# Kernel tuning notes

Measured on AMD Instinct MI355X. Metric: run time of the kernel, lower is better.

The kernel has to match this reference:

```python
import jax, jax.numpy as jnp
import numpy as np

N = 10000      # nodes
E = 160000     # edges (before self-loops)
IN = 256
NEG_SLOPE = 0.2  # PyG GATConv default


def gat_layer(x, src, dst, W, a_src, a_dst, bias, heads, concat, n):
    # x: [n, in_dim]; W: [in_dim, heads*C]; a_src/a_dst: [heads, C]
    C = W.shape[1] // heads
    h = (x @ W).reshape(n, heads, C)                      # [n,H,C]
    es = jnp.einsum('nhc,hc->nh', h, a_src)               # [n,H]
    ed = jnp.einsum('nhc,hc->nh', h, a_dst)               # [n,H]
    e = jax.nn.leaky_relu(es[src] + ed[dst], NEG_SLOPE)   # [E,H]
    # segment softmax over destination node (every node has a self-loop)
    emax = jax.ops.segment_max(e, dst, num_segments=n)    # [n,H]
    al = jnp.exp(e - emax[dst])                           # [E,H]
    den = jax.ops.segment_sum(al, dst, num_segments=n)    # [n,H]
    al = al / den[dst]
    out = jax.ops.segment_sum(h[src] * al[:, :, None], dst, num_segments=n)  # [n,H,C]
    out = out.reshape(n, heads * C) if concat else out.mean(axis=1)
    return out + bias


def setup_inputs() -> dict:
    key = jax.random.key(0)
    ks = jax.random.split(key, 16)
    s = 0.05
    p = lambda k, shp: jax.random.normal(k, shp, dtype=jnp.float32) * s
    return {
        'x': jax.random.normal(ks[0], (N, IN), dtype=jnp.float32),
        'edge_index': jax.random.randint(ks[1], (2, E), 0, N, dtype=jnp.int64),
        'proj_w': p(ks[2], (IN, 512)), 'proj_b': jnp.zeros((512,), jnp.float32),
        'w1': p(ks[3], (512, 4 * 512)),  'as1': p(ks[4], (4, 512)), 'ad1': p(ks[5], (4, 512)),  'b1': jnp.zeros((2048,), jnp.float32),
        'w2': p(ks[6], (2048, 4 * 512)), 'as2': p(ks[7], (4, 512)), 'ad2': p(ks[8], (4, 512)),  'b2': jnp.zeros((2048,), jnp.float32),
        'w3': p(ks[9], (2048, 2 * 512)), 'as3': p(ks[10], (2, 512)), 'ad3': p(ks[11], (2, 512)), 'b3': jnp.zeros((512,), jnp.float32),
    }


def reference(x, edge_index, proj_w, proj_b, w1, as1, ad1, b1,
              w2, as2, ad2, b2, w3, as3, ad3, b3):
    n = x.shape[0]
    loops = jnp.arange(n, dtype=edge_index.dtype)
    src = jnp.concatenate([edge_index[0], loops])   # PyG add_self_loops=True
    dst = jnp.concatenate([edge_index[1], loops])
    h = x @ proj_w + proj_b                         # dropout is identity in eval
    h = gat_layer(h, src, dst, w1, as1, ad1, b1, 4, True, n)
    h = jax.nn.elu(h)
    h = gat_layer(h, src, dst, w2, as2, ad2, b2, 4, True, n)
    h = jax.nn.elu(h)
    h = gat_layer(h, src, dst, w3, as3, ad3, b3, 2, False, n)
    return h
```

## Files before the change

kernel.cpp:

```cpp
#include <hip/hip_runtime.h>
#include <hip/hip_bf16.h>
#include <math.h>

#define CDIV(a,b) (((a)+(b)-1)/(b))

typedef __bf16  bf16x8 __attribute__((ext_vector_type(8)));
typedef float   f32x4  __attribute__((ext_vector_type(4)));
typedef unsigned short u16x8 __attribute__((ext_vector_type(8)));
typedef unsigned short u16x4 __attribute__((ext_vector_type(4)));

__device__ __forceinline__ float bf2f(unsigned short u) {
    union { unsigned int i; float f; } x; x.i = ((unsigned int)u) << 16; return x.f;
}
__device__ __forceinline__ unsigned short f2bf(float f) {
    union { float f; unsigned int i; } x; x.f = f;
    unsigned int r = x.i + 0x7fff + ((x.i >> 16) & 1);
    return (unsigned short)(r >> 16);
}

__device__ __forceinline__ void bfx8_cvt(u16x8 v, float f[8]) {
    union { u16x8 v; unsigned d[4]; } u; u.v = v;
#pragma unroll
    for (int q = 0; q < 4; q++) {
        f[2*q]   = __uint_as_float(u.d[q] << 16);
        f[2*q+1] = __uint_as_float(u.d[q] & 0xffff0000u);
    }
}
__device__ __forceinline__ void bfx4_cvt(u16x4 v, float f[4]) {
    union { u16x4 v; unsigned d[2]; } u; u.v = v;
#pragma unroll
    for (int q = 0; q < 2; q++) {
        f[2*q]   = __uint_as_float(u.d[q] << 16);
        f[2*q+1] = __uint_as_float(u.d[q] & 0xffff0000u);
    }
}
__device__ __forceinline__ float elu_fast(float v) {
    return (v > 0.f) ? v : (__expf(v) - 1.f);
}

__global__ void hist_kernel(const int* __restrict__ ei, int* __restrict__ deg,
                            int E, int Et) {
    int e = blockIdx.x * blockDim.x + threadIdx.x;
    if (e >= Et) return;
    int d = (e < E) ? ei[E + e] : (e - E);
    atomicAdd(&deg[d], 1);
}

__global__ void scan_kernel(const int* __restrict__ deg, int* __restrict__ off, int n) {
    __shared__ int wsum[16];
    __shared__ int carry_s;
    int t = threadIdx.x, lane = t & 63, wv = t >> 6;
    if (t == 0) carry_s = 0;
    __syncthreads();
    for (int base = 0; base < n; base += 1024) {
        int v = (base + t < n) ? deg[base + t] : 0;
        int x = v;
#pragma unroll
        for (int o = 1; o < 64; o <<= 1) {
            int y = __shfl_up(x, o);
            if (lane >= o) x += y;
        }
        if (lane == 63) wsum[wv] = x;
        __syncthreads();
        if (wv == 0 && lane < 16) {
            int s = wsum[lane];
#pragma unroll
            for (int o = 1; o < 16; o <<= 1) {
                int y = __shfl_up(s, o);
                if (lane >= o) s += y;
            }
            wsum[lane] = s;
        }
        __syncthreads();
        int wprev = (wv == 0) ? 0 : wsum[wv - 1];
        int incl = carry_s + wprev + x;
        if (base + t < n) off[base + t] = incl - v;
        __syncthreads();
        if (t == 1023) carry_s = incl;
        __syncthreads();
    }
    if (t == 0) off[n] = carry_s;
}

__global__ void scatter_kernel(const int* __restrict__ ei, const int* __restrict__ off,
                               int* __restrict__ cur, int* __restrict__ csr,
                               int E, int Et) {
    int e = blockIdx.x * blockDim.x + threadIdx.x;
    if (e >= Et) return;
    int s, d;
    if (e < E) { s = ei[e]; d = ei[E + e]; } else { s = e - E; d = s; }
    int pos = off[d] + atomicAdd(&cur[d], 1);
    csr[pos] = s;
}

__global__ void prep_t_kernel(const float* __restrict__ wa, __hip_bfloat16* __restrict__ wta,
                              const float* __restrict__ wb, __hip_bfloat16* __restrict__ wtb,
                              const float* __restrict__ wc, __hip_bfloat16* __restrict__ wtc,
                              int t0, int t1, int t2) {
    __shared__ float tile[32][33];
    int bid = blockIdx.x;
    const float* w; __hip_bfloat16* wt; int K, N, r;
    if (bid < t0)      { w = wa; wt = wta; K = 512;  N = 2048; r = bid; }
    else if (bid < t1) { w = wb; wt = wtb; K = 2048; N = 2048; r = bid - t0; }
    else               { w = wc; wt = wtc; K = 2048; N = 1024; r = bid - t1; }
    (void)t2;
    int kt = K >> 5;
    int kb = (r % kt) * 32, nb = (r / kt) * 32;
    int tx = threadIdx.x & 31, ty = threadIdx.x >> 5;
    for (int i = ty; i < 32; i += 8)
        tile[i][tx] = w[(size_t)(kb + i) * N + nb + tx];
    __syncthreads();
    for (int i = ty; i < 32; i += 8)
        wt[(size_t)(nb + i) * K + kb + tx] = __float2bfloat16(tile[tx][i]);
}

__global__ void cvt2_kernel(const float* __restrict__ a, __hip_bfloat16* __restrict__ ao,
                            int na4,
                            const float* __restrict__ b, __hip_bfloat16* __restrict__ bo,
                            int nb4) {
    int i = blockIdx.x * blockDim.x + threadIdx.x;
    const float* src; __hip_bfloat16* dst; int idx;
    if (i < na4) { src = a; dst = ao; idx = i * 4; }
    else if (i < na4 + nb4) { src = b; dst = bo; idx = (i - na4) * 4; }
    else return;
    float4 v = *(const float4*)(src + idx);
    dst[idx + 0] = __float2bfloat16(v.x);
    dst[idx + 1] = __float2bfloat16(v.y);
    dst[idx + 2] = __float2bfloat16(v.z);
    dst[idx + 3] = __float2bfloat16(v.w);
}

__global__ void beff_kernel(const float* __restrict__ pb, const float* __restrict__ w1,
                            float* __restrict__ beff, int N) {
    int j  = blockIdx.x * 256 + threadIdx.x;
    int k0 = blockIdx.y * 64;
    float s = 0.f;
#pragma unroll
    for (int k = 0; k < 64; k++)
        s = fmaf(pb[k0 + k], w1[(size_t)(k0 + k) * N + j], s);
    atomicAdd(&beff[j], s);
}

__global__ void va_kernel(const __hip_bfloat16* __restrict__ w_efft,
                          const float* __restrict__ b_eff,
                          const float* __restrict__ as1, const float* __restrict__ ad1,
                          const float* __restrict__ b1,
                          float* __restrict__ va, float* __restrict__ cvec,
                          float* __restrict__ b1s) {
    int j = blockIdx.x, t = threadIdx.x;
    if (j == 8) {
        for (int i = t; i < 2048; i += 256) b1s[i] = b_eff[i] + b1[i];
        return;
    }
    int h = j & 3;
    const float* a = ((j < 4) ? as1 : ad1) + h * 512;
    __shared__ float aLDS[512];
    __shared__ float red[256];
    for (int c = t; c < 512; c += 256) aLDS[c] = a[c];
    __syncthreads();
    float acc = 0.f;
    const unsigned short* wb = (const unsigned short*)w_efft + (size_t)h * 512 * 256 + t;
    for (int c = 0; c < 512; c++)
        acc = fmaf(aLDS[c], bf2f(wb[(size_t)c * 256]), acc);
    va[j * 256 + t] = acc;
    float cp = b_eff[h * 512 + t] * aLDS[t] + b_eff[h * 512 + 256 + t] * aLDS[256 + t];
    red[t] = cp;
    __syncthreads();
    for (int s = 128; s > 0; s >>= 1) {
        if (t < s) red[t] += red[t + s];
        __syncthreads();
    }
    if (t == 0) cvec[j] = red[0];
}

__global__ void es1_kernel(const __hip_bfloat16* __restrict__ x_bf,
                           const float* __restrict__ va, const float* __restrict__ cvec,
                           float* __restrict__ es, float* __restrict__ ed) {
    int node = blockIdx.x, l = threadIdx.x;
    u16x4 xv = *(const u16x4*)((const unsigned short*)x_bf + (size_t)node * 256 + l * 4);
    float xf[4];
    bfx4_cvt(xv, xf);
    float dot[8];
#pragma unroll
    for (int j = 0; j < 8; j++) {
        float4 v = *(const float4*)(va + j * 256 + l * 4);
        dot[j] = xf[0] * v.x + xf[1] * v.y + xf[2] * v.z + xf[3] * v.w;
    }
#pragma unroll
    for (int j = 0; j < 8; j++)
        for (int o = 32; o; o >>= 1) dot[j] += __shfl_down(dot[j], o);
    if (l == 0) {
#pragma unroll
        for (int h = 0; h < 4; h++) {
            es[node * 4 + h] = dot[h] + cvec[h];
            ed[node * 4 + h] = dot[4 + h] + cvec[4 + h];
        }
    }
}

__global__ __launch_bounds__(256) void alpha4_kernel(
    const float* __restrict__ es, const float* __restrict__ ed,
    const int* __restrict__ csr, const int* __restrict__ off,
    float4* __restrict__ al4, int n)
{
    int d = blockIdx.x * 4 + (threadIdx.x >> 6);
    if (d >= n) return;
    int lane = threadIdx.x & 63;
    int beg = off[d], end = off[d + 1];
    float edd[4], den[4];
#pragma unroll
    for (int h = 0; h < 4; h++) { edd[h] = ed[d * 4 + h]; den[h] = 0.f; }
    for (int i = beg + lane; i < end; i += 64) {
        int s = csr[i];
#pragma unroll
        for (int h = 0; h < 4; h++) {
            float e = es[s * 4 + h] + edd[h];
            e = (e > 0.f) ? e : 0.2f * e;
            den[h] += __expf(e);
        }
    }
#pragma unroll
    for (int h = 0; h < 4; h++) {
        for (int o = 32; o; o >>= 1) den[h] += __shfl_down(den[h], o);
        den[h] = __shfl(den[h], 0);
        den[h] = 1.f / den[h];
    }
    for (int i = beg + lane; i < end; i += 64) {
        int s = csr[i];
        float a[4];
#pragma unroll
        for (int h = 0; h < 4; h++) {
            float e = es[s * 4 + h] + edd[h];
            e = (e > 0.f) ? e : 0.2f * e;
            a[h] = __expf(e) * den[h];
        }
        al4[i] = make_float4(a[0], a[1], a[2], a[3]);
    }
}

__global__ __launch_bounds__(256) void agg1x_kernel(
    const __hip_bfloat16* __restrict__ x_bf, const float4* __restrict__ al4,
    const int* __restrict__ csr, const int* __restrict__ off,
    __hip_bfloat16* __restrict__ z)
{
    __shared__ float red[4][1024];
    int d = blockIdx.x, t = threadIdx.x;
    int w = t >> 6, l = t & 63;
    int c0 = l * 4;
    int beg = off[d], end = off[d + 1];
    float acc[4][4] = {};
    const unsigned short* xb = (const unsigned short*)x_bf;

    for (int i = beg + w; i < end; i += 4) {
        int s = csr[i];
        float4 a = al4[i];
        u16x4 xv = *(const u16x4*)(xb + (size_t)s * 256 + c0);
        float xf[4];
        bfx4_cvt(xv, xf);
#pragma unroll
        for (int k = 0; k < 4; k++) {
            acc[k][0] = fmaf(a.x, xf[k], acc[k][0]);
            acc[k][1] = fmaf(a.y, xf[k], acc[k][1]);
            acc[k][2] = fmaf(a.z, xf[k], acc[k][2]);
            acc[k][3] = fmaf(a.w, xf[k], acc[k][3]);
        }
    }
#pragma unroll
    for (int h = 0; h < 4; h++)
#pragma unroll
        for (int k = 0; k < 4; k++)
            red[w][h * 256 + c0 + k] = acc[k][h];
    __syncthreads();
    unsigned short* zb = (unsigned short*)z + (size_t)d * 1024;
#pragma unroll
    for (int q = 0; q < 4; q++) {
        int m = t + q * 256;
        float v = red[0][m] + red[1][m] + red[2][m] + red[3][m];
        zb[m] = f2bf(v);
    }
}

__device__ __forceinline__ void gload16(void* lds, const void* g) {
    __builtin_amdgcn_global_load_lds(
        (const __attribute__((address_space(1))) void*)g,
        (__attribute__((address_space(3))) void*)lds, 16, 0, 0);
}

__global__ __launch_bounds__(256) void gemm_bf16_kernel(
    const __hip_bfloat16* __restrict__ A,
    const __hip_bfloat16* __restrict__ BT,
    const float* __restrict__ bias,
    __hip_bfloat16* __restrict__ Cb,
    int M, int N, int K, int lda, int hko, int do_elu,
    int MB, int NB, int XT, int NBH)
{
    __shared__ __align__(16) __hip_bfloat16 As[128 * 32];
    __shared__ __align__(16) __hip_bfloat16 Bs[128 * 32];

    const int bid  = blockIdx.x;
    const int xcd  = bid & 7;
    const int slot = bid >> 3;
    const int per_yh = XT * NBH;
    const int yh    = slot / per_yh;
    const int rem   = slot - yh * per_yh;
    const int x_sub = rem / NBH;
    const int ys    = rem - x_sub * NBH;
    const int yb    = yh * NBH + ys;
    const int xb    = xcd * XT + x_sub;
    if (xb >= MB || yb >= NB) return;

    const int tid = threadIdx.x;
    const int m0 = xb * 128, n0 = yb * 128;
    const int w = tid >> 6, l = tid & 63;
    const int wm = (w & 1) * 64, wn = (w >> 1) * 64;
    const int lm = l & 15, lq = l >> 4;

    f32x4 acc[4][4] = {};

    const int arow = tid >> 2;
    const int acol = (tid & 3) * 8;
    const __hip_bfloat16* Ag = A + (size_t)(m0 + arow) * lda + acol + (n0 >> 9) * hko;
    const __hip_bfloat16* Bg = BT + (size_t)(n0 + arow) * K + acol;
    char* AsW = (char*)As + (w << 10);
    char* BsW = (char*)Bs + (w << 10);

    for (int k0 = 0; k0 < K; k0 += 32) {
        gload16(AsW,        Ag + k0);
        gload16(AsW + 4096, Ag + (size_t)64 * lda + k0);
        gload16(BsW,        Bg + k0);
        gload16(BsW + 4096, Bg + (size_t)64 * K + k0);
        __syncthreads();
        bf16x8 af[4], bfr[4];
#pragma unroll
        for (int i = 0; i < 4; i++)
            af[i] = *(const bf16x8*)(As + (wm + i * 16 + lm) * 32 + lq * 8);
#pragma unroll
        for (int j = 0; j < 4; j++)
            bfr[j] = *(const bf16x8*)(Bs + (wn + j * 16 + lm) * 32 + lq * 8);
#pragma unroll
        for (int i = 0; i < 4; i++)
#pragma unroll
            for (int j = 0; j < 4; j++)
                acc[i][j] = __builtin_amdgcn_mfma_f32_16x16x32_bf16(
                    af[i], bfr[j], acc[i][j], 0, 0, 0);
        __syncthreads();
    }

#pragma unroll
    for (int i = 0; i < 4; i++) {
        int rb = m0 + wm + i * 16 + lq * 4;
#pragma unroll
        for (int r = 0; r < 4; r++) {
            int row = rb + r;
            if (row >= M) continue;
#pragma unroll
            for (int j = 0; j < 4; j++) {
                int col = n0 + wn + j * 16 + lm;
                float v = acc[i][j][r];
                if (bias) v += bias[col];
                if (do_elu) v = elu_fast(v);
                Cb[(size_t)row * N + col] = __float2bfloat16(v);
            }
        }
    }
}

__global__ __launch_bounds__(512, 2) void gemm256_kernel(
    const __hip_bfloat16* __restrict__ A,
    const __hip_bfloat16* __restrict__ BT,
    __hip_bfloat16* __restrict__ Cb,
    int M, int N, int K, int MT, int nfull)
{
    __shared__ __align__(16) char smem[131072];
    const int NT = K >> 6;

    const int cpx  = gridDim.x >> 3;
    const int bid  = blockIdx.x;
    const int slot = (bid & 7) * cpx + (bid >> 3);
    int mt, ntl;
    if (slot < nfull) { mt = slot % MT; ntl = slot / MT; }
    else              { ntl = nfull / MT; mt = (nfull % MT) + (slot - nfull); }
    const int m0 = mt << 8, n0 = ntl << 8;

    const int tid = threadIdx.x;
    const int w  = tid >> 6, l = tid & 63;
    const int wr = w >> 2, wc = w & 3;
    const int lm = l & 15, lq = l >> 4;

    const int srow = tid >> 3;
    const int scol = ((l & 7) << 3) ^ ((l >> 3) << 3);
    const __hip_bfloat16* As0 = A  + (size_t)(m0 + srow) * K + scol;
    const __hip_bfloat16* Bs0 = BT + (size_t)(n0 + srow) * K + scol;
    const size_t rs64  = (size_t)64  * K;
    const size_t rs128 = (size_t)128 * K;
    char* const stA = smem +          ((size_t)w << 10);
    char* const stB = smem + 65536 +  ((size_t)w << 10);

    auto STAGE_A = [&](int par, int hf, int tt) {
        char* d = stA + (((par << 1) | hf) << 14);
        const __hip_bfloat16* s = As0 + (size_t)hf * rs128 + (tt << 6);
        gload16(d,        s);
        gload16(d + 8192, s + rs64);
    };
    auto STAGE_B = [&](int par, int hf, int tt) {
        char* d = stB + (((par << 1) | hf) << 14);
        const __hip_bfloat16* s = Bs0 + (size_t)hf * rs128 + (tt << 6);
        gload16(d,        s);
        gload16(d + 8192, s + rs64);
    };

    const int roff = lm << 7;
    const int xm   = (lm & 7) << 4;
    const int off0 = (lq << 4) ^ xm;
    const int off1 = off0 ^ 64;
    const int bsel = 65536 + ((wc & 1) << 13);

    f32x4  acc[8][4] = {};
    bf16x8 af[8][2];
    bf16x8 bfr[2][2];

    STAGE_A(0, 0, 0); STAGE_A(0, 1, 0);
    STAGE_B(0, 0, 0); STAGE_B(0, 1, 0);
    STAGE_A(1, 0, 1); STAGE_A(1, 1, 1);
    asm volatile("s_waitcnt vmcnt(4)" ::: "memory");
    __builtin_amdgcn_s_barrier();

    for (int t = 0; t < NT; ++t) {
        const int par = t & 1;
        const char* aS = smem + (((par << 1) | wr)        << 14) + roff;
        const char* bS = smem + (((par << 1) | (wc >> 1)) << 14) + bsel + roff;

#pragma unroll
        for (int i = 0; i < 4; ++i) {
            af[i][0] = *(const bf16x8*)(aS + i * 2048 + off0);
            af[i][1] = *(const bf16x8*)(aS + i * 2048 + off1);
        }
#pragma unroll
        for (int j = 0; j < 2; ++j) {
            bfr[j][0] = *(const bf16x8*)(bS + j * 2048 + off0);
            bfr[j][1] = *(const bf16x8*)(bS + j * 2048 + off1);
        }
        if (t + 1 < NT) STAGE_B(par ^ 1, 0, t + 1);
        __builtin_amdgcn_s_barrier();
        asm volatile("s_waitcnt lgkmcnt(0)" ::: "memory");
        __builtin_amdgcn_sched_barrier(0);
        __builtin_amdgcn_s_setprio(1);
#pragma unroll
        for (int i = 0; i < 4; ++i)
#pragma unroll
            for (int j = 0; j < 2; ++j) {
                acc[i][j] = __builtin_amdgcn_mfma_f32_16x16x32_bf16(af[i][0], bfr[j][0], acc[i][j], 0, 0, 0);
                acc[i][j] = __builtin_amdgcn_mfma_f32_16x16x32_bf16(af[i][1], bfr[j][1], acc[i][j], 0, 0, 0);
            }
        __builtin_amdgcn_s_setprio(0);
        __builtin_amdgcn_s_barrier();

#pragma unroll
        for (int i = 4; i < 8; ++i) {
            af[i][0] = *(const bf16x8*)(aS + i * 2048 + off0);
            af[i][1] = *(const bf16x8*)(aS + i * 2048 + off1);
        }
        if (t + 1 < NT) STAGE_B(par ^ 1, 1, t + 1);
        __builtin_amdgcn_s_barrier();
        asm volatile("s_waitcnt lgkmcnt(0)" ::: "memory");
        __builtin_amdgcn_sched_barrier(0);
        __builtin_amdgcn_s_setprio(1);
#pragma unroll
        for (int i = 4; i < 8; ++i)
#pragma unroll
            for (int j = 0; j < 2; ++j) {
                acc[i][j] = __builtin_amdgcn_mfma_f32_16x16x32_bf16(af[i][0], bfr[j][0], acc[i][j], 0, 0, 0);
                acc[i][j] = __builtin_amdgcn_mfma_f32_16x16x32_bf16(af[i][1], bfr[j][1], acc[i][j], 0, 0, 0);
            }
        __builtin_amdgcn_s_setprio(0);
        __builtin_amdgcn_s_barrier();

#pragma unroll
        for (int j = 0; j < 2; ++j) {
            bfr[j][0] = *(const bf16x8*)(bS + (j + 2) * 2048 + off0);
            bfr[j][1] = *(const bf16x8*)(bS + (j + 2) * 2048 + off1);
        }
        if (t + 2 < NT) STAGE_A(par, 0, t + 2);
        __builtin_amdgcn_s_barrier();
        asm volatile("s_waitcnt lgkmcnt(0)" ::: "memory");
        __builtin_amdgcn_sched_barrier(0);
        __builtin_amdgcn_s_setprio(1);
#pragma unroll
        for (int i = 0; i < 4; ++i)
#pragma unroll
            for (int j = 0; j < 2; ++j) {
                acc[i][j + 2] = __builtin_amdgcn_mfma_f32_16x16x32_bf16(af[i][0], bfr[j][0], acc[i][j + 2], 0, 0, 0);
                acc[i][j + 2] = __builtin_amdgcn_mfma_f32_16x16x32_bf16(af[i][1], bfr[j][1], acc[i][j + 2], 0, 0, 0);
            }
        __builtin_amdgcn_s_setprio(0);
        __builtin_amdgcn_s_barrier();

        if (t + 2 < NT) STAGE_A(par, 1, t + 2);
        __builtin_amdgcn_s_barrier();
        __builtin_amdgcn_sched_barrier(0);
        __builtin_amdgcn_s_setprio(1);
#pragma unroll
        for (int i = 4; i < 8; ++i)
#pragma unroll
            for (int j = 0; j < 2; ++j) {
                acc[i][j + 2] = __builtin_amdgcn_mfma_f32_16x16x32_bf16(af[i][0], bfr[j][0], acc[i][j + 2], 0, 0, 0);
                acc[i][j + 2] = __builtin_amdgcn_mfma_f32_16x16x32_bf16(af[i][1], bfr[j][1], acc[i][j + 2], 0, 0, 0);
            }
        __builtin_amdgcn_s_setprio(0);
        if (t + 2 < NT)      { asm volatile("s_waitcnt vmcnt(4)" ::: "memory"); }
        else if (t + 1 < NT) { asm volatile("s_waitcnt vmcnt(0)" ::: "memory"); }
        __builtin_amdgcn_s_barrier();
    }

#pragma unroll
    for (int i = 0; i < 8; ++i) {
        int rb = m0 + wr * 128 + i * 16 + lq * 4;
#pragma unroll
        for (int r = 0; r < 4; ++r) {
            int row = rb + r;
            if (row >= M) continue;
#pragma unroll
            for (int j = 0; j < 4; ++j) {
                int col = n0 + wc * 64 + j * 16 + lm;
                Cb[(size_t)row * N + col] = __float2bfloat16(acc[i][j][r]);
            }
        }
    }
}

__global__ __launch_bounds__(256, 2) void gemm128_kernel(
    const __hip_bfloat16* __restrict__ A,
    const __hip_bfloat16* __restrict__ BT,
    __hip_bfloat16* __restrict__ Cb,
    int M, int N, int K, int mode, int RT)
{
    __shared__ __align__(16) char smem[65536];
    const int NT = K >> 6;

    const int cpx  = gridDim.x >> 3;
    const int bid  = blockIdx.x;
    const int slot = (bid & 7) * cpx + (bid >> 3);
    int r, c;
    if (mode == 0) { r = slot % RT; c = slot / RT; }
    else {
        if (slot < 96) { c = 12 + slot / 48; r = 32 + slot % 48; }
        else           { int u = slot - 96; c = 14 + u / 80; r = u % 80; }
    }
    const int m0 = r << 7, n0 = c << 7;

    const int tid = threadIdx.x;
    const int w = tid >> 6, l = tid & 63;
    const int wm = (w & 1) << 6, wn = (w >> 1) << 6;
    const int lm = l & 15, lq = l >> 4;

    const int srow = tid >> 3;
    const int scol = (((tid & 7) ^ ((tid >> 3) & 7)) << 3);
    const __hip_bfloat16* Ag = A  + (size_t)(m0 + srow) * K + scol;
    const __hip_bfloat16* Bg = BT + (size_t)(n0 + srow) * K + scol;
    const size_t rs32 = (size_t)32 * K;
    char* const dA = smem +         ((size_t)w << 10);
    char* const dB = smem + 16384 + ((size_t)w << 10);

    auto STAGE = [&](int par, int tt) {
        char* pa = dA + (par << 15);
        char* pb = dB + (par << 15);
        const __hip_bfloat16* sa = Ag + (tt << 6);
        const __hip_bfloat16* sb = Bg + (tt << 6);
#pragma unroll
        for (int s = 0; s < 4; ++s) {
            gload16(pa + (s << 12), sa + (size_t)s * rs32);
            gload16(pb + (s << 12), sb + (size_t)s * rs32);
        }
    };

    const int roff = lm << 7;
    const int off0 = (lq << 4) ^ ((lm & 7) << 4);
    const int off1 = off0 ^ 64;

    f32x4 acc[4][4] = {};

    STAGE(0, 0);
    asm volatile("s_waitcnt vmcnt(0)" ::: "memory");
    __builtin_amdgcn_s_barrier();

    for (int t = 0; t < NT; ++t) {
        const int par = t & 1;
        if (t + 1 < NT) STAGE(par ^ 1, t + 1);
        const char* aS = smem + (par << 15) +         wm * 128 + roff;
        const char* bS = smem + (par << 15) + 16384 + wn * 128 + roff;
        bf16x8 af[4][2], bfr[4][2];
#pragma unroll
        for (int i = 0; i < 4; ++i) {
            af[i][0]  = *(const bf16x8*)(aS + i * 2048 + off0);
            af[i][1]  = *(const bf16x8*)(aS + i * 2048 + off1);
            bfr[i][0] = *(const bf16x8*)(bS + i * 2048 + off0);
            bfr[i][1] = *(const bf16x8*)(bS + i * 2048 + off1);
        }
        asm volatile("s_waitcnt lgkmcnt(0)" ::: "memory");
        __builtin_amdgcn_sched_barrier(0);
        __builtin_amdgcn_s_setprio(1);
#pragma unroll
        for (int i = 0; i < 4; ++i)
#pragma unroll
            for (int j = 0; j < 4; ++j) {
                acc[i][j] = __builtin_amdgcn_mfma_f32_16x16x32_bf16(af[i][0], bfr[j][0], acc[i][j], 0, 0, 0);
                acc[i][j] = __builtin_amdgcn_mfma_f32_16x16x32_bf16(af[i][1], bfr[j][1], acc[i][j], 0, 0, 0);
            }
        __builtin_amdgcn_s_setprio(0);
        if (t + 1 < NT) asm volatile("s_waitcnt vmcnt(0)" ::: "memory");
        __builtin_amdgcn_s_barrier();
    }

#pragma unroll
    for (int i = 0; i < 4; ++i) {
        int rb = m0 + wm + i * 16 + lq * 4;
#pragma unroll
        for (int r2 = 0; r2 < 4; ++r2) {
            int row = rb + r2;
            if (row >= M) continue;
#pragma unroll
            for (int j = 0; j < 4; ++j) {
                int col = n0 + wn + j * 16 + lm;
                Cb[(size_t)row * N + col] = __float2bfloat16(acc[i][j][r2]);
            }
        }
    }
}

__global__ void esed_kernel(const __hip_bfloat16* __restrict__ h,
                            const float* __restrict__ a_src,
                            const float* __restrict__ a_dst,
                            float* __restrict__ es, float* __restrict__ ed, int H) {
    int nidx = blockIdx.x;
    int t = threadIdx.x;
    int head = t >> 6, lane = t & 63;
    const unsigned short* hp =
        (const unsigned short*)h + (size_t)nidx * H * 512 + head * 512 + lane * 8;
    const float* sp = a_src + head * 512 + lane * 8;
    const float* dp = a_dst + head * 512 + lane * 8;
    u16x8 hv = *(const u16x8*)hp;
    float4 s0 = *(const float4*)sp, s1 = *(const float4*)(sp + 4);
    float4 d0 = *(const float4*)dp, d1 = *(const float4*)(dp + 4);
    float hf[8];
    bfx8_cvt(hv, hf);
    float s = hf[0]*s0.x + hf[1]*s0.y + hf[2]*s0.z + hf[3]*s0.w
            + hf[4]*s1.x + hf[5]*s1.y + hf[6]*s1.z + hf[7]*s1.w;
    float d = hf[0]*d0.x + hf[1]*d0.y + hf[2]*d0.z + hf[3]*d0.w
            + hf[4]*d1.x + hf[5]*d1.y + hf[6]*d1.z + hf[7]*d1.w;
    for (int o = 32; o; o >>= 1) { s += __shfl_down(s, o); d += __shfl_down(d, o); }
    if (lane == 0) { es[nidx * H + head] = s; ed[nidx * H + head] = d; }
}

template<int H, int SHIFT>
__global__ __launch_bounds__(256) void alpharec_kernel(
    const float* __restrict__ es, const float* __restrict__ ed,
    const int* __restrict__ csr, const int* __restrict__ off,
    uint2* __restrict__ rec, int n)
{
    int d = blockIdx.x * 4 + (threadIdx.x >> 6);
    if (d >= n) return;
    int lane = threadIdx.x & 63;
    int beg = off[d], end = off[d + 1];
    float edd[H], den[H];
#pragma unroll
    for (int h = 0; h < H; h++) { edd[h] = ed[d * H + h]; den[h] = 0.f; }
    for (int i = beg + lane; i < end; i += 64) {
        int s = csr[i];
#pragma unroll
        for (int h = 0; h < H; h++) {
            float e = es[s * H + h] + edd[h];
            e = (e > 0.f) ? e : 0.2f * e;
            den[h] += __expf(e);
        }
    }
#pragma unroll
    for (int h = 0; h < H; h++) {
        for (int o = 32; o; o >>= 1) den[h] += __shfl_down(den[h], o);
        den[h] = __shfl(den[h], 0);
        den[h] = 1.f / den[h];
    }
    for (int i = beg + lane; i < end; i += 64) {
        int s = csr[i];
        unsigned obytes = ((unsigned)s) << SHIFT;
#pragma unroll
        for (int h = 0; h < H; h++) {
            float e = es[s * H + h] + edd[h];
            e = (e > 0.f) ? e : 0.2f * e;
            float a = __expf(e) * den[h];
            rec[(size_t)i * H + h] = make_uint2(obytes, __float_as_uint(a));
        }
    }
}

__global__ __launch_bounds__(256) void agg2s_kernel(
    const __hip_bfloat16* __restrict__ h, const uint2* __restrict__ rec,
    const int* __restrict__ off, const float* __restrict__ bias,
    __hip_bfloat16* __restrict__ outB, int n)
{
    const int bid   = blockIdx.x;
    const int slice = bid & 7;
    const int head  = slice >> 1;
    const int wvs   = (bid >> 3) * 4 + (threadIdx.x >> 6);
    const int lane  = threadIdx.x & 63;
    const int half  = lane >> 5;
    const int c0    = slice * 256 + (lane & 31) * 8;
    const unsigned c0b = (unsigned)c0 * 2;
    const char* hb = (const char*)h;
    float bv[8];
#pragma unroll
    for (int k = 0; k < 8; k++) bv[k] = bias[c0 + k];

    for (int d = wvs; d < n; d += 1024) {
        int beg = off[d], end = off[d + 1];
        float acc[8] = {0.f, 0.f, 0.f, 0.f, 0.f, 0.f, 0.f, 0.f};
        int i = beg + half;
        for (; i + 2 < end; i += 4) {
            uint2 r0 = rec[i * 4 + head];
            uint2 r1 = rec[(i + 2) * 4 + head];
            u16x8 v0 = *(const u16x8*)(hb + (size_t)(r0.x + c0b));
            u16x8 v1 = *(const u16x8*)(hb + (size_t)(r1.x + c0b));
            float a0 = __uint_as_float(r0.y);
            float a1 = __uint_as_float(r1.y);
            float f0[8], f1[8];
            bfx8_cvt(v0, f0);
            bfx8_cvt(v1, f1);
#pragma unroll
            for (int k = 0; k < 8; k++) acc[k] = fmaf(a0, f0[k], acc[k]);
#pragma unroll
            for (int k = 0; k < 8; k++) acc[k] = fmaf(a1, f1[k], acc[k]);
        }
        for (; i < end; i += 2) {
            uint2 r0 = rec[i * 4 + head];
            u16x8 v0 = *(const u16x8*)(hb + (size_t)(r0.x + c0b));
            float a0 = __uint_as_float(r0.y);
            float f0[8];
            bfx8_cvt(v0, f0);
#pragma unroll
            for (int k = 0; k < 8; k++) acc[k] = fmaf(a0, f0[k], acc[k]);
        }
#pragma unroll
        for (int k = 0; k < 8; k++) acc[k] += __shfl_xor(acc[k], 32);
        if (half == 0) {
            u16x8 ov;
#pragma unroll
            for (int k = 0; k < 8; k++) {
                float v = elu_fast(acc[k] + bv[k]);
                ov[k] = f2bf(v);
            }
            *(u16x8*)((unsigned short*)outB + (size_t)d * 2048 + c0) = ov;
        }
    }
}

__global__ __launch_bounds__(256) void agg3s_kernel(
    const __hip_bfloat16* __restrict__ h, const uint2* __restrict__ rec,
    const int* __restrict__ off, float* __restrict__ part, int n)
{
    const int bid   = blockIdx.x;
    const int xcd   = bid & 7;
    const int slice = xcd >> 1;
    const int head  = slice >> 1;
    const int sb    = ((bid >> 3) << 1) | (xcd & 1);
    const int wvs   = sb * 4 + (threadIdx.x >> 6);
    const int lane  = threadIdx.x & 63;
    const int half  = lane >> 5;
    const int c0    = slice * 256 + (lane & 31) * 8;
    const unsigned c0b = (unsigned)c0 * 2;
    const char* hb = (const char*)h;

    for (int d = wvs; d < n; d += 2048) {
        int beg = off[d], end = off[d + 1];
        float acc[8] = {0.f, 0.f, 0.f, 0.f, 0.f, 0.f, 0.f, 0.f};
        int i = beg + half;
        for (; i + 2 < end; i += 4) {
            uint2 r0 = rec[i * 2 + head];
            uint2 r1 = rec[(i + 2) * 2 + head];
            u16x8 v0 = *(const u16x8*)(hb + (size_t)(r0.x + c0b));
            u16x8 v1 = *(const u16x8*)(hb + (size_t)(r1.x + c0b));
            float a0 = __uint_as_float(r0.y);
            float a1 = __uint_as_float(r1.y);
            float f0[8], f1[8];
            bfx8_cvt(v0, f0);
            bfx8_cvt(v1, f1);
#pragma unroll
            for (int k = 0; k < 8; k++) acc[k] = fmaf(a0, f0[k], acc[k]);
#pragma unroll
            for (int k = 0; k < 8; k++) acc[k] = fmaf(a1, f1[k], acc[k]);
        }
        for (; i < end; i += 2) {
            uint2 r0 = rec[i * 2 + head];
            u16x8 v0 = *(const u16x8*)(hb + (size_t)(r0.x + c0b));
            float a0 = __uint_as_float(r0.y);
            float f0[8];
            bfx8_cvt(v0, f0);
#pragma unroll
            for (int k = 0; k < 8; k++) acc[k] = fmaf(a0, f0[k], acc[k]);
        }
#pragma unroll
        for (int k = 0; k < 8; k++) acc[k] += __shfl_xor(acc[k], 32);
        if (half == 0) {
            float* pp = part + (size_t)d * 1024 + c0;
            *(float4*)pp       = make_float4(acc[0], acc[1], acc[2], acc[3]);
            *(float4*)(pp + 4) = make_float4(acc[4], acc[5], acc[6], acc[7]);
        }
    }
}

__global__ void comb3_kernel(const float* __restrict__ part,
                             const float* __restrict__ b3,
                             float* __restrict__ out, int n) {
    int idx = blockIdx.x * 256 + threadIdx.x;
    if (idx >= n * 128) return;
    int d = idx >> 7, c = (idx & 127) * 4;
    float4 p0 = *(const float4*)(part + (size_t)d * 1024 + c);
    float4 p1 = *(const float4*)(part + (size_t)d * 1024 + 512 + c);
    float4 bb = *(const float4*)(b3 + c);
    float4 o;
    o.x = 0.5f * (p0.x + p1.x) + bb.x;
    o.y = 0.5f * (p0.y + p1.y) + bb.y;
    o.z = 0.5f * (p0.z + p1.z) + bb.z;
    o.w = 0.5f * (p0.w + p1.w) + bb.w;
    *(float4*)(out + (size_t)d * 512 + c) = o;
}

extern "C" void kernel_launch(void* const* d_in, const int* in_sizes, int n_in,
                              void* d_out, int out_size, void* d_ws, size_t ws_size,
                              hipStream_t stream) {
    const float* x      = (const float*)d_in[0];
    const int*   ei     = (const int*)  d_in[1];
    const float* proj_w = (const float*)d_in[2];
    const float* proj_b = (const float*)d_in[3];
    const float* w1  = (const float*)d_in[4];
    const float* as1 = (const float*)d_in[5];
    const float* ad1 = (const float*)d_in[6];
    const float* b1  = (const float*)d_in[7];
    const float* w2  = (const float*)d_in[8];
    const float* as2 = (const float*)d_in[9];
    const float* ad2 = (const float*)d_in[10];
    const float* b2  = (const float*)d_in[11];
    const float* w3  = (const float*)d_in[12];
    const float* as3 = (const float*)d_in[13];
    const float* ad3 = (const float*)d_in[14];
    const float* b3  = (const float*)d_in[15];

    const int n    = in_sizes[0] / 256;
    const int E    = in_sizes[1] / 2;
    const int Et   = E + n;
    const int MB   = CDIV(n, 128);
    const int MB2  = CDIV(n, 256);
    const int Mpad = MB2 * 256;
    const int XT   = CDIV(MB, 8);

    char* p = (char*)d_ws;
    auto carve = [&](size_t bytes) {
        void* r = (void*)p;
        p += (bytes + 255) & ~(size_t)255;
        return r;
    };
    __hip_bfloat16* h_bf    = (__hip_bfloat16*)carve((size_t)Mpad * 2048 * sizeof(__hip_bfloat16));
    __hip_bfloat16* act_bf  = (__hip_bfloat16*)carve((size_t)Mpad * 2048 * sizeof(__hip_bfloat16));
    __hip_bfloat16* x_bf    = (__hip_bfloat16*)carve((size_t)Mpad * 256 * sizeof(__hip_bfloat16));
    __hip_bfloat16* pw_bf   = (__hip_bfloat16*)carve((size_t)256 * 512 * sizeof(__hip_bfloat16));
    __hip_bfloat16* w1t     = (__hip_bfloat16*)carve((size_t)2048 * 512 * sizeof(__hip_bfloat16));
    __hip_bfloat16* w2t     = (__hip_bfloat16*)carve((size_t)2048 * 2048 * sizeof(__hip_bfloat16));
    __hip_bfloat16* w3t     = (__hip_bfloat16*)carve((size_t)1024 * 2048 * sizeof(__hip_bfloat16));
    __hip_bfloat16* w_efft  = (__hip_bfloat16*)carve((size_t)2048 * 256 * sizeof(__hip_bfloat16));
    float* b_eff = (float*)carve((size_t)2048 * sizeof(float));
    float* b1s   = (float*)carve((size_t)2048 * sizeof(float));
    float* va    = (float*)carve((size_t)8 * 256 * sizeof(float));
    float* cvec  = (float*)carve((size_t)8 * sizeof(float));
    float* es  = (float*)carve((size_t)n * 4 * sizeof(float));
    float* ed  = (float*)carve((size_t)n * 4 * sizeof(float));
    uint2* rec = (uint2*)carve((size_t)Et * 4 * sizeof(uint2));
    int* deg = (int*)carve((size_t)2 * n * sizeof(int));
    int* cur = deg + n;
    int* off = (int*)carve((size_t)(n + 1) * sizeof(int));
    int* csr = (int*)carve((size_t)Et * sizeof(int));
    __hip_bfloat16* z_bf = h_bf;
    float* part = (float*)act_bf;
    float4* al4 = (float4*)rec;
    (void)ws_size; (void)n_in;

    hipMemsetAsync(deg, 0, 2 * n * sizeof(int), stream);
    hipMemsetAsync(b_eff, 0, 2048 * sizeof(float), stream);
    hist_kernel<<<CDIV(Et, 256), 256, 0, stream>>>(ei, deg, E, Et);
    scan_kernel<<<1, 1024, 0, stream>>>(deg, off, n);
    scatter_kernel<<<CDIV(Et, 256), 256, 0, stream>>>(ei, off, cur, csr, E, Et);

    const int t0 = (512 / 32) * (2048 / 32);
    const int t1 = t0 + (2048 / 32) * (2048 / 32);
    const int t2 = t1 + (2048 / 32) * (1024 / 32);
    prep_t_kernel<<<t2, 256, 0, stream>>>(w1, w1t, w2, w2t, w3, w3t, t0, t1, t2);
    const int na4 = 256 * 512 / 4, nb4 = n * 256 / 4;
    cvt2_kernel<<<CDIV(na4 + nb4, 256), 256, 0, stream>>>(proj_w, pw_bf, na4, x, x_bf, nb4);

    gemm_bf16_kernel<<<8 * 2 * 2, 256, 0, stream>>>(
        w1t, pw_bf, nullptr, w_efft, 2048, 256, 512, 512, 0, 0, 16, 2, 2, 2);
    beff_kernel<<<dim3(2048 / 256, 512 / 64), 256, 0, stream>>>(proj_b, w1, b_eff, 2048);

    va_kernel<<<9, 256, 0, stream>>>(w_efft, b_eff, as1, ad1, b1, va, cvec, b1s);

    es1_kernel<<<n, 64, 0, stream>>>(x_bf, va, cvec, es, ed);
    alpha4_kernel<<<CDIV(n, 4), 256, 0, stream>>>(es, ed, csr, off, al4, n);
    agg1x_kernel<<<n, 256, 0, stream>>>(x_bf, al4, csr, off, z_bf);
    gemm_bf16_kernel<<<8 * XT * 16, 256, 0, stream>>>(
        z_bf, w_efft, b1s, act_bf, n, 2048, 256, 1024, 256, 1, MB, 16, XT, 16);

    gemm256_kernel<<<256, 512, 0, stream>>>(act_bf, w2t, h_bf, n, 2048, 2048, 40, 240);
    gemm128_kernel<<<256, 256, 0, stream>>>(act_bf, w2t, h_bf, n, 2048, 2048, 1, 0);
    esed_kernel<<<n, 4 * 64, 0, stream>>>(h_bf, as2, ad2, es, ed, 4);
    alpharec_kernel<4, 12><<<CDIV(n, 4), 256, 0, stream>>>(es, ed, csr, off, rec, n);
    agg2s_kernel<<<2048, 256, 0, stream>>>(h_bf, rec, off, b2, act_bf, n);

    gemm128_kernel<<<640, 256, 0, stream>>>(act_bf, w3t, h_bf, n, 1024, 2048, 0, 80);
    esed_kernel<<<n, 2 * 64, 0, stream>>>(h_bf, as3, ad3, es, ed, 2);
    alpharec_kernel<2, 11><<<CDIV(n, 4), 256, 0, stream>>>(es, ed, csr, off, rec, n);
    agg3s_kernel<<<2048, 256, 0, stream>>>(h_bf, rec, off, part, n);
    comb3_kernel<<<CDIV(n * 128, 256), 256, 0, stream>>>(part, b3, (float*)d_out, n);
}
```

Measured before the change: 572.7 us.

## Fuse layer-1 softmax into aggregation and fold head-mean into layer-3 aggregation

Removes the separate alpha4 kernel: agg1x now computes the per-destination softmax denominator with a block reduction and recomputes the attention weights inline, so the float4 alpha array is never written or read back. In layer 3, each wave now accumulates both heads for its output columns, applies the 0.5 mean and bias, and writes the final output directly. This drops the partial buffer and the comb3 kernel. The costs are recomputed exps, doubled gather work per wave in agg3, and a changed grid mapping that drops the XCD-aware slicing, with the grid-stride loop now stepping by 4096.

```diff
diff --git a/kernel.cpp b/kernel.cpp
--- a/kernel.cpp
+++ b/kernel.cpp
@@ -198,71 +198,67 @@
     }
 }
 
-__global__ __launch_bounds__(256) void alpha4_kernel(
-    const float* __restrict__ es, const float* __restrict__ ed,
-    const int* __restrict__ csr, const int* __restrict__ off,
-    float4* __restrict__ al4, int n)
-{
-    int d = blockIdx.x * 4 + (threadIdx.x >> 6);
-    if (d >= n) return;
-    int lane = threadIdx.x & 63;
-    int beg = off[d], end = off[d + 1];
-    float edd[4], den[4];
-#pragma unroll
-    for (int h = 0; h < 4; h++) { edd[h] = ed[d * 4 + h]; den[h] = 0.f; }
-    for (int i = beg + lane; i < end; i += 64) {
-        int s = csr[i];
-#pragma unroll
-        for (int h = 0; h < 4; h++) {
-            float e = es[s * 4 + h] + edd[h];
-            e = (e > 0.f) ? e : 0.2f * e;
-            den[h] += __expf(e);
-        }
-    }
-#pragma unroll
-    for (int h = 0; h < 4; h++) {
-        for (int o = 32; o; o >>= 1) den[h] += __shfl_down(den[h], o);
-        den[h] = __shfl(den[h], 0);
-        den[h] = 1.f / den[h];
-    }
-    for (int i = beg + lane; i < end; i += 64) {
-        int s = csr[i];
-        float a[4];
-#pragma unroll
-        for (int h = 0; h < 4; h++) {
-            float e = es[s * 4 + h] + edd[h];
-            e = (e > 0.f) ? e : 0.2f * e;
-            a[h] = __expf(e) * den[h];
-        }
-        al4[i] = make_float4(a[0], a[1], a[2], a[3]);
-    }
-}
-
 __global__ __launch_bounds__(256) void agg1x_kernel(
-    const __hip_bfloat16* __restrict__ x_bf, const float4* __restrict__ al4,
-    const int* __restrict__ csr, const int* __restrict__ off,
-    __hip_bfloat16* __restrict__ z)
+    const __hip_bfloat16* __restrict__ x_bf, const float* __restrict__ es,
+    const float* __restrict__ ed, const int* __restrict__ csr,
+    const int* __restrict__ off, __hip_bfloat16* __restrict__ z)
 {
     __shared__ float red[4][1024];
+    __shared__ float denS[4][4];
     int d = blockIdx.x, t = threadIdx.x;
     int w = t >> 6, l = t & 63;
     int c0 = l * 4;
     int beg = off[d], end = off[d + 1];
+    float4 edv = *(const float4*)(ed + d * 4);
+    float edd[4] = {edv.x, edv.y, edv.z, edv.w};
+
+    float den[4] = {0.f, 0.f, 0.f, 0.f};
+    for (int i = beg + t; i < end; i += 256) {
+        int s = csr[i];
+        float4 ev = *(const float4*)(es + s * 4);
+        float e0 = ev.x + edd[0]; e0 = (e0 > 0.f) ? e0 : 0.2f * e0;
+        float e1 = ev.y + edd[1]; e1 = (e1 > 0.f) ? e1 : 0.2f * e1;
+        float e2 = ev.z + edd[2]; e2 = (e2 > 0.f) ? e2 : 0.2f * e2;
+        float e3 = ev.w + edd[3]; e3 = (e3 > 0.f) ? e3 : 0.2f * e3;
+        den[0] += __expf(e0); den[1] += __expf(e1);
+        den[2] += __expf(e2); den[3] += __expf(e3);
+    }
+#pragma unroll
+    for (int h = 0; h < 4; h++)
+        for (int o = 32; o; o >>= 1) den[h] += __shfl_down(den[h], o);
+    if (l == 0) {
+#pragma unroll
+        for (int h = 0; h < 4; h++) denS[w][h] = den[h];
+    }
+    __syncthreads();
+    float inv[4];
+#pragma unroll
+    for (int h = 0; h < 4; h++)
+        inv[h] = 1.f / (denS[0][h] + denS[1][h] + denS[2][h] + denS[3][h]);
+
     float acc[4][4] = {};
     const unsigned short* xb = (const unsigned short*)x_bf;
-
     for (int i = beg + w; i < end; i += 4) {
         int s = csr[i];
-        float4 a = al4[i];
+        float4 ev = *(const float4*)(es + s * 4);
+        float a[4];
+        {
+            float e0 = ev.x + edd[0]; e0 = (e0 > 0.f) ? e0 : 0.2f * e0;
+            float e1 = ev.y + edd[1]; e1 = (e1 > 0.f) ? e1 : 0.2f * e1;
+            float e2 = ev.z + edd[2]; e2 = (e2 > 0.f) ? e2 : 0.2f * e2;
+            float e3 = ev.w + edd[3]; e3 = (e3 > 0.f) ? e3 : 0.2f * e3;
+            a[0] = __expf(e0) * inv[0]; a[1] = __expf(e1) * inv[1];
+            a[2] = __expf(e2) * inv[2]; a[3] = __expf(e3) * inv[3];
+        }
         u16x4 xv = *(const u16x4*)(xb + (size_t)s * 256 + c0);
         float xf[4];
         bfx4_cvt(xv, xf);
 #pragma unroll
         for (int k = 0; k < 4; k++) {
-            acc[k][0] = fmaf(a.x, xf[k], acc[k][0]);
-            acc[k][1] = fmaf(a.y, xf[k], acc[k][1]);
-            acc[k][2] = fmaf(a.z, xf[k], acc[k][2]);
-            acc[k][3] = fmaf(a.w, xf[k], acc[k][3]);
+            acc[k][0] = fmaf(a[0], xf[k], acc[k][0]);
+            acc[k][1] = fmaf(a[1], xf[k], acc[k][1]);
+            acc[k][2] = fmaf(a[2], xf[k], acc[k][2]);
+            acc[k][3] = fmaf(a[3], xf[k], acc[k][3]);
         }
     }
 #pragma unroll
@@ -754,73 +750,75 @@
 
 __global__ __launch_bounds__(256) void agg3s_kernel(
     const __hip_bfloat16* __restrict__ h, const uint2* __restrict__ rec,
-    const int* __restrict__ off, float* __restrict__ part, int n)
+    const int* __restrict__ off, const float* __restrict__ b3,
+    float* __restrict__ out, int n)
 {
     const int bid   = blockIdx.x;
-    const int xcd   = bid & 7;
-    const int slice = xcd >> 1;
-    const int head  = slice >> 1;
-    const int sb    = ((bid >> 3) << 1) | (xcd & 1);
+    const int slice = bid & 1;
+    const int sb    = bid >> 1;
     const int wvs   = sb * 4 + (threadIdx.x >> 6);
     const int lane  = threadIdx.x & 63;
     const int half  = lane >> 5;
     const int c0    = slice * 256 + (lane & 31) * 8;
     const unsigned c0b = (unsigned)c0 * 2;
     const char* hb = (const char*)h;
-
-    for (int d = wvs; d < n; d += 2048) {
+    float bv[8];
+#pragma unroll
+    for (int k = 0; k < 8; k++) bv[k] = b3[c0 + k];
+
+    for (int d = wvs; d < n; d += 4096) {
         int beg = off[d], end = off[d + 1];
         float acc[8] = {0.f, 0.f, 0.f, 0.f, 0.f, 0.f, 0.f, 0.f};
         int i = beg + half;
         for (; i + 2 < end; i += 4) {
-            uint2 r0 = rec[i * 2 + head];
-            uint2 r1 = rec[(i + 2) * 2 + head];
-            u16x8 v0 = *(const u16x8*)(hb + (size_t)(r0.x + c0b));
-            u16x8 v1 = *(const u16x8*)(hb + (size_t)(r1.x + c0b));
-            float a0 = __uint_as_float(r0.y);
-            float a1 = __uint_as_float(r1.y);
-            float f0[8], f1[8];
-            bfx8_cvt(v0, f0);
-            bfx8_cvt(v1, f1);
-#pragma unroll
-            for (int k = 0; k < 8; k++) acc[k] = fmaf(a0, f0[k], acc[k]);
-#pragma unroll
-            for (int k = 0; k < 8; k++) acc[k] = fmaf(a1, f1[k], acc[k]);
+            uint4 r0 = *(const uint4*)(rec + (size_t)i * 2);
+            uint4 r1 = *(const uint4*)(rec + (size_t)(i + 2) * 2);
+            u16x8 v00 = *(const u16x8*)(hb + (size_t)(r0.x + c0b));
+            u16x8 v01 = *(const u16x8*)(hb + (size_t)(r0.x + 1024 + c0b));
+            u16x8 v10 = *(const u16x8*)(hb + (size_t)(r1.x + c0b));
+            u16x8 v11 = *(const u16x8*)(hb + (size_t)(r1.x + 1024 + c0b));
+            float a00 = __uint_as_float(r0.y), a01 = __uint_as_float(r0.w);
+            float a10 = __uint_as_float(r1.y), a11 = __uint_as_float(r1.w);
+            float f[8];
+            bfx8_cvt(v00, f);
+#pragma unroll
+            for (int k = 0; k < 8; k++) acc[k] = fmaf(a00, f[k], acc[k]);
+            bfx8_cvt(v01, f);
+#pragma unroll
+            for (int k = 0; k < 8; k++) acc[k] = fmaf(a01, f[k], acc[k]);
+            bfx8_cvt(v10, f);
+#pragma unroll
+            for (int k = 0; k < 8; k++) acc[k] = fmaf(a10, f[k], acc[k]);
+            bfx8_cvt(v11, f);
+#pragma unroll
+            for (int k = 0; k < 8; k++) acc[k] = fmaf(a11, f[k], acc[k]);
         }
         for (; i < end; i += 2) {
-            uint2 r0 = rec[i * 2 + head];
-            u16x8 v0 = *(const u16x8*)(hb + (size_t)(r0.x + c0b));
-            float a0 = __uint_as_float(r0.y);
-            float f0[8];
-            bfx8_cvt(v0, f0);
-#pragma unroll
-            for (int k = 0; k < 8; k++) acc[k] = fmaf(a0, f0[k], acc[k]);
+            uint4 r0 = *(const uint4*)(rec + (size_t)i * 2);
+            u16x8 v00 = *(const u16x8*)(hb + (size_t)(r0.x + c0b));
+            u16x8 v01 = *(const u16x8*)(hb + (size_t)(r0.x + 1024 + c0b));
+            float a00 = __uint_as_float(r0.y), a01 = __uint_as_float(r0.w);
+            float f[8];
+            bfx8_cvt(v00, f);
+#pragma unroll
+            for (int k = 0; k < 8; k++) acc[k] = fmaf(a00, f[k], acc[k]);
+            bfx8_cvt(v01, f);
+#pragma unroll
+            for (int k = 0; k < 8; k++) acc[k] = fmaf(a01, f[k], acc[k]);
         }
 #pragma unroll
         for (int k = 0; k < 8; k++) acc[k] += __shfl_xor(acc[k], 32);
         if (half == 0) {
-            float* pp = part + (size_t)d * 1024 + c0;
-            *(float4*)pp       = make_float4(acc[0], acc[1], acc[2], acc[3]);
-            *(float4*)(pp + 4) = make_float4(acc[4], acc[5], acc[6], acc[7]);
-        }
-    }
-}
-
-__global__ void comb3_kernel(const float* __restrict__ part,
-                             const float* __restrict__ b3,
-                             float* __restrict__ out, int n) {
-    int idx = blockIdx.x * 256 + threadIdx.x;
-    if (idx >= n * 128) return;
-    int d = idx >> 7, c = (idx & 127) * 4;
-    float4 p0 = *(const float4*)(part + (size_t)d * 1024 + c);
-    float4 p1 = *(const float4*)(part + (size_t)d * 1024 + 512 + c);
-    float4 bb = *(const float4*)(b3 + c);
-    float4 o;
-    o.x = 0.5f * (p0.x + p1.x) + bb.x;
-    o.y = 0.5f * (p0.y + p1.y) + bb.y;
-    o.z = 0.5f * (p0.z + p1.z) + bb.z;
-    o.w = 0.5f * (p0.w + p1.w) + bb.w;
-    *(float4*)(out + (size_t)d * 512 + c) = o;
+            float* op = out + (size_t)d * 512 + c0;
+            float4 o0, o1;
+            o0.x = 0.5f * acc[0] + bv[0]; o0.y = 0.5f * acc[1] + bv[1];
+            o0.z = 0.5f * acc[2] + bv[2]; o0.w = 0.5f * acc[3] + bv[3];
+            o1.x = 0.5f * acc[4] + bv[4]; o1.y = 0.5f * acc[5] + bv[5];
+            o1.z = 0.5f * acc[6] + bv[6]; o1.w = 0.5f * acc[7] + bv[7];
+            *(float4*)op       = o0;
+            *(float4*)(op + 4) = o1;
+        }
+    }
 }
 
 extern "C" void kernel_launch(void* const* d_in, const int* in_sizes, int n_in,
@@ -877,8 +875,6 @@
     int* off = (int*)carve((size_t)(n + 1) * sizeof(int));
     int* csr = (int*)carve((size_t)Et * sizeof(int));
     __hip_bfloat16* z_bf = h_bf;
-    float* part = (float*)act_bf;
-    float4* al4 = (float4*)rec;
     (void)ws_size; (void)n_in;
 
     hipMemsetAsync(deg, 0, 2 * n * sizeof(int), stream);
@@ -901,8 +897,7 @@
     va_kernel<<<9, 256, 0, stream>>>(w_efft, b_eff, as1, ad1, b1, va, cvec, b1s);
 
     es1_kernel<<<n, 64, 0, stream>>>(x_bf, va, cvec, es, ed);
-    alpha4_kernel<<<CDIV(n, 4), 256, 0, stream>>>(es, ed, csr, off, al4, n);
-    agg1x_kernel<<<n, 256, 0, stream>>>(x_bf, al4, csr, off, z_bf);
+    agg1x_kernel<<<n, 256, 0, stream>>>(x_bf, es, ed, csr, off, z_bf);
     gemm_bf16_kernel<<<8 * XT * 16, 256, 0, stream>>>(
         z_bf, w_efft, b1s, act_bf, n, 2048, 256, 1024, 256, 1, MB, 16, XT, 16);
 
@@ -915,6 +910,5 @@
     gemm128_kernel<<<640, 256, 0, stream>>>(act_bf, w3t, h_bf, n, 1024, 2048, 0, 80);
     esed_kernel<<<n, 2 * 64, 0, stream>>>(h_bf, as3, ad3, es, ed, 2);
     alpharec_kernel<2, 11><<<CDIV(n, 4), 256, 0, stream>>>(es, ed, csr, off, rec, n);
-    agg3s_kernel<<<2048, 256, 0, stream>>>(h_bf, rec, off, part, n);
-    comb3_kernel<<<CDIV(n * 128, 256), 256, 0, stream>>>(part, b3, (float*)d_out, n);
-}
+    agg3s_kernel<<<2048, 256, 0, stream>>>(h_bf, rec, off, b3, (float*)d_out, n);
+}
```

Result: no change. 581.7 us (+1.6%).
